# Optimization experiments

Hardware: AMD Instinct MI355X
Metric: run time of the kernel (lower is better)

Reference implementation:

```python
import jax, jax.numpy as jnp
from jax import lax
import numpy as np

KERNEL_SIZE = 5
GROUP_SIZE = 40
GMAX = 160                      # g sampled in [0, GMAX)
MAX_ITERS = (GMAX - 1) // GROUP_SIZE   # static upper bound on |g|//group_size = 3
B = 4096
D = 8192


def _circ_conv(x, k):
    # x: [1, B, D], k: [B, K] -> grouped (depthwise) circular conv1d, groups=B
    pad = KERNEL_SIZE - 1
    left = pad // 2
    xp = jnp.pad(x, ((0, 0), (0, 0), (left, pad - left)), mode='wrap')
    return lax.conv_general_dilated(
        xp, k[:, None, :], window_strides=(1,), padding='VALID',
        feature_group_count=k.shape[0], dimension_numbers=('NCH', 'OIH', 'NCH'))


def setup_inputs() -> dict:
    key = jax.random.key(0)
    k1, k2, k3 = jax.random.split(key, 3)
    x = jax.random.normal(k1, (B, D), dtype=jnp.float32)
    g = jax.random.randint(k2, (B,), 0, GMAX, dtype=jnp.int32)
    kernels = jax.random.normal(k3, (2 * GROUP_SIZE + 1, KERNEL_SIZE), dtype=jnp.float32)
    return {"x": x, "g": g, "kernels": kernels}


def reference(x, g, kernels):
    G = GROUP_SIZE
    xc = x[None]                          # [1, B, D]  (x.view(-1,1,D).permute(1,0,2))
    sign = jnp.sign(g)                    # [B]
    iters = jnp.abs(g) // G               # [B] data-dependent per-sample loop count
    max_it = jnp.max(iters)               # dynamic max over the batch
    max_k = kernels[sign * G + G]         # [B, K]
    id_k = kernels[G]                     # [K] learned 'identity' kernel
    # true delta kernel: exact no-op under circular pad, used for steps past max_it
    delta = jnp.zeros((KERNEL_SIZE,), x.dtype).at[(KERNEL_SIZE - 1) // 2].set(1.0)

    h = xc
    for i in range(MAX_ITERS):            # static bound; delta makes extra steps no-ops
        inactive = jnp.where(i < max_it, id_k, delta)          # [K]
        k_i = jnp.where((i < iters)[:, None], max_k, inactive[None, :])  # [B, K]
        h = _circ_conv(h, k_i)
    rem = jnp.abs(g) % G
    fin_k = kernels[rem * sign + G]       # [B, K]
    out = _circ_conv(h, fin_k)            # [1, B, D]
    return jnp.transpose(out, (1, 0, 2))  # [B, 1, D]
```

## Files before the change

kernel.cpp:

```cpp
#include <hip/hip_runtime.h>

#define BB 4096
#define DD 8192
#define KK 5
#define GS 40
#define MAXIT 3
#define EFF 17
#define CHUNK 2048
#define C4 (CHUNK/4)
#define DF4 (DD/4)

typedef float vf4 __attribute__((ext_vector_type(4)));

__device__ __forceinline__ int iabs(int a) { return a < 0 ? -a : a; }

__global__ __launch_bounds__(256) void k_max_it(const int* __restrict__ g,
                                                int* __restrict__ ws) {
    __shared__ int red[256];
    int t = threadIdx.x;
    int m = 0;
    for (int i = t; i < BB; i += 256) m = max(m, iabs(g[i]));
    red[t] = m;
    __syncthreads();
    for (int s = 128; s > 0; s >>= 1) {
        if (t < s) red[t] = max(red[t], red[t + s]);
        __syncthreads();
    }
    if (t == 0) ws[0] = red[0] / GS;
}

__global__ __launch_bounds__(256) void k_conv(const float* __restrict__ x,
                                              const int* __restrict__ g,
                                              const float* __restrict__ kernels,
                                              const int* __restrict__ ws,
                                              float* __restrict__ out) {
    __shared__ float lds[CHUNK + 16];
    float4* ldsv = (float4*)lds;

    const int bi   = blockIdx.x;
    const int b    = bi >> 2;
    const int ch   = bi & 3;
    const int t    = threadIdx.x;
    const int c0f4 = ch * C4;

    const float4* xr = (const float4*)(x + (size_t)b * DD);

    ldsv[2 + t]       = xr[c0f4 + t];
    ldsv[2 + t + 256] = xr[c0f4 + t + 256];
    if (t == 0) {
        ldsv[0] = xr[(c0f4 - 2) & (DF4 - 1)];
        ldsv[1] = xr[(c0f4 - 1) & (DF4 - 1)];
    } else if (t == 1) {
        ldsv[514] = xr[(c0f4 + C4)     & (DF4 - 1)];
        ldsv[515] = xr[(c0f4 + C4 + 1) & (DF4 - 1)];
    }

    const int gv    = g[b];
    const int sign  = gv > 0 ? 1 : (gv < 0 ? -1 : 0);
    const int a     = iabs(gv);
    const int iters = a / GS;
    const int rem   = a % GS;
    const int max_it = ws[0];

    float maxk[KK], idk[KK], fink[KK];
    const float* mk = kernels + (size_t)(sign * GS + GS) * KK;
    const float* ik = kernels + (size_t)GS * KK;
    const float* fk = kernels + (size_t)(rem * sign + GS) * KK;
#pragma unroll
    for (int j = 0; j < KK; ++j) { maxk[j] = mk[j]; idk[j] = ik[j]; fink[j] = fk[j]; }

    float e[EFF], ne[EFF];
#pragma unroll
    for (int m = 0; m < EFF; ++m) e[m] = 0.f;
    e[0] = 1.f;
    int len = 1;
    for (int i = 0; i < MAXIT; ++i) {
        float kk5[KK];
        if (i < iters) {
#pragma unroll
            for (int j = 0; j < KK; ++j) kk5[j] = maxk[j];
        } else if (i < max_it) {
#pragma unroll
            for (int j = 0; j < KK; ++j) kk5[j] = idk[j];
        } else {
#pragma unroll
            for (int j = 0; j < KK; ++j) kk5[j] = (j == (KK - 1) / 2) ? 1.f : 0.f;
        }
#pragma unroll
        for (int m = 0; m < EFF; ++m) ne[m] = 0.f;
        for (int m = 0; m < len; ++m)
#pragma unroll
            for (int j = 0; j < KK; ++j) ne[m + j] += e[m] * kk5[j];
        len += KK - 1;
#pragma unroll
        for (int m = 0; m < EFF; ++m) e[m] = ne[m];
    }
#pragma unroll
    for (int m = 0; m < EFF; ++m) ne[m] = 0.f;
    for (int m = 0; m < len; ++m)
#pragma unroll
        for (int j = 0; j < KK; ++j) ne[m + j] += e[m] * fink[j];
#pragma unroll
    for (int m = 0; m < EFF; ++m) e[m] = ne[m];

    __syncthreads();

    vf4* outr = (vf4*)(out + (size_t)b * DD);
#pragma unroll
    for (int jb = 0; jb < 2; ++jb) {
        const int v = jb * 256 + t;
        float f[EFF + 3];
#pragma unroll
        for (int q = 0; q < 5; ++q) {
            float4 val = ldsv[v + q];
            f[q * 4 + 0] = val.x; f[q * 4 + 1] = val.y;
            f[q * 4 + 2] = val.z; f[q * 4 + 3] = val.w;
        }
        float oc[4];
#pragma unroll
        for (int c = 0; c < 4; ++c) {
            float s = 0.f;
#pragma unroll
            for (int m = 0; m < EFF; ++m) s += e[m] * f[c + m];
            oc[c] = s;
        }
        vf4 o;
        o.x = oc[0]; o.y = oc[1]; o.z = oc[2]; o.w = oc[3];
        __builtin_nontemporal_store(o, outr + c0f4 + v);
    }
}

extern "C" void kernel_launch(void* const* d_in, const int* in_sizes, int n_in,
                              void* d_out, int out_size, void* d_ws, size_t ws_size,
                              hipStream_t stream) {
    const float* x       = (const float*)d_in[0];
    const int*   g       = (const int*)d_in[1];
    const float* kernels = (const float*)d_in[2];
    float*       out     = (float*)d_out;
    int*         ws      = (int*)d_ws;

    k_max_it<<<1, 256, 0, stream>>>(g, ws);
    k_conv<<<BB * (DD / CHUNK), 256, 0, stream>>>(x, g, kernels, ws, out);
}
```

Baseline: 236.8 us.

## Precompute composed per-row 17-tap kernels in a separate pass

Adds a small kernel that computes the batch max and each row's composed 17-tap filter once, writing the results to workspace. The main conv kernel then loads five float4 values instead of recomputing the filter composition in every one of the four chunk blocks per row. The loop-based composition is also replaced with fully unrolled fixed-length templates. The old path is kept as a fallback when the workspace is too small, and each of the 16 compose blocks redoes the full max reduction over g.

```diff
diff --git a/kernel.cpp b/kernel.cpp
--- a/kernel.cpp
+++ b/kernel.cpp
@@ -9,31 +9,92 @@
 #define CHUNK 2048
 #define C4 (CHUNK/4)
 #define DF4 (DD/4)
+#define EPAD 20
+#define WS_OFF 64
 
 typedef float vf4 __attribute__((ext_vector_type(4)));
 
 __device__ __forceinline__ int iabs(int a) { return a < 0 ? -a : a; }
 
-__global__ __launch_bounds__(256) void k_max_it(const int* __restrict__ g,
-                                                int* __restrict__ ws) {
+template<int LEN>
+__device__ __forceinline__ void compose5(float* e, const float* k5) {
+    float ne[LEN + KK - 1];
+#pragma unroll
+    for (int m = 0; m < LEN + KK - 1; ++m) ne[m] = 0.f;
+#pragma unroll
+    for (int m = 0; m < LEN; ++m)
+#pragma unroll
+        for (int j = 0; j < KK; ++j) ne[m + j] += e[m] * k5[j];
+#pragma unroll
+    for (int m = 0; m < LEN + KK - 1; ++m) e[m] = ne[m];
+}
+
+__device__ __forceinline__ void pick5(int i, int iters, int max_it,
+                                      const float* maxk, const float* idk,
+                                      float* k5) {
+#pragma unroll
+    for (int j = 0; j < KK; ++j)
+        k5[j] = (i < iters) ? maxk[j]
+              : ((i < max_it) ? idk[j] : ((j == (KK - 1) / 2) ? 1.f : 0.f));
+}
+
+__global__ __launch_bounds__(256) void k_compose(const int* __restrict__ g,
+                                                 const float* __restrict__ kernels,
+                                                 float* __restrict__ wsE) {
     __shared__ int red[256];
-    int t = threadIdx.x;
+    const int t = threadIdx.x;
+
+    const int4* g4 = (const int4*)g;
     int m = 0;
-    for (int i = t; i < BB; i += 256) m = max(m, iabs(g[i]));
+    for (int i = t; i < BB / 4; i += 256) {
+        int4 v = g4[i];
+        m = max(m, max(max(iabs(v.x), iabs(v.y)), max(iabs(v.z), iabs(v.w))));
+    }
     red[t] = m;
     __syncthreads();
     for (int s = 128; s > 0; s >>= 1) {
         if (t < s) red[t] = max(red[t], red[t + s]);
         __syncthreads();
     }
-    if (t == 0) ws[0] = red[0] / GS;
-}
-
-__global__ __launch_bounds__(256) void k_conv(const float* __restrict__ x,
-                                              const int* __restrict__ g,
-                                              const float* __restrict__ kernels,
-                                              const int* __restrict__ ws,
-                                              float* __restrict__ out) {
+    const int max_it = red[0] / GS;
+
+    const int r  = blockIdx.x * 256 + t;
+    const int gv = g[r];
+    const int sign  = gv > 0 ? 1 : (gv < 0 ? -1 : 0);
+    const int a     = iabs(gv);
+    const int iters = a / GS;
+    const int rem   = a % GS;
+
+    const float* mk = kernels + (size_t)(sign * GS + GS) * KK;
+    const float* ik = kernels + (size_t)GS * KK;
+    const float* fk = kernels + (size_t)(rem * sign + GS) * KK;
+    float maxk[KK], idk[KK], fink[KK];
+#pragma unroll
+    for (int j = 0; j < KK; ++j) { maxk[j] = mk[j]; idk[j] = ik[j]; fink[j] = fk[j]; }
+
+    float e[EPAD];
+#pragma unroll
+    for (int q = 0; q < EPAD; ++q) e[q] = 0.f;
+    e[0] = 1.f;
+
+    float k5[KK];
+    pick5(0, iters, max_it, maxk, idk, k5); compose5<1>(e, k5);
+    pick5(1, iters, max_it, maxk, idk, k5); compose5<5>(e, k5);
+    pick5(2, iters, max_it, maxk, idk, k5); compose5<9>(e, k5);
+    compose5<13>(e, fink);
+
+    vf4* dst = (vf4*)(wsE + (size_t)r * EPAD);
+    vf4 o0; o0.x = e[0];  o0.y = e[1];  o0.z = e[2];  o0.w = e[3];
+    vf4 o1; o1.x = e[4];  o1.y = e[5];  o1.z = e[6];  o1.w = e[7];
+    vf4 o2; o2.x = e[8];  o2.y = e[9];  o2.z = e[10]; o2.w = e[11];
+    vf4 o3; o3.x = e[12]; o3.y = e[13]; o3.z = e[14]; o3.w = e[15];
+    vf4 o4; o4.x = e[16]; o4.y = e[17]; o4.z = e[18]; o4.w = e[19];
+    dst[0] = o0; dst[1] = o1; dst[2] = o2; dst[3] = o3; dst[4] = o4;
+}
+
+__global__ __launch_bounds__(256) void k_conv_pre(const float* __restrict__ x,
+                                                  const float* __restrict__ wsE,
+                                                  float* __restrict__ out) {
     __shared__ float lds[CHUNK + 16];
     float4* ldsv = (float4*)lds;
 
@@ -55,6 +116,82 @@
         ldsv[515] = xr[(c0f4 + C4 + 1) & (DF4 - 1)];
     }
 
+    const float4* ev = (const float4*)(wsE + (size_t)b * EPAD);
+    float4 e0 = ev[0], e1 = ev[1], e2 = ev[2], e3 = ev[3], e4 = ev[4];
+    float e[EFF] = { e0.x, e0.y, e0.z, e0.w,
+                     e1.x, e1.y, e1.z, e1.w,
+                     e2.x, e2.y, e2.z, e2.w,
+                     e3.x, e3.y, e3.z, e3.w,
+                     e4.x };
+
+    __syncthreads();
+
+    vf4* outr = (vf4*)(out + (size_t)b * DD);
+#pragma unroll
+    for (int jb = 0; jb < 2; ++jb) {
+        const int v = jb * 256 + t;
+        float f[EFF + 3];
+#pragma unroll
+        for (int q = 0; q < 5; ++q) {
+            float4 val = ldsv[v + q];
+            f[q * 4 + 0] = val.x; f[q * 4 + 1] = val.y;
+            f[q * 4 + 2] = val.z; f[q * 4 + 3] = val.w;
+        }
+        float oc[4];
+#pragma unroll
+        for (int c = 0; c < 4; ++c) {
+            float s = 0.f;
+#pragma unroll
+            for (int m = 0; m < EFF; ++m) s += e[m] * f[c + m];
+            oc[c] = s;
+        }
+        vf4 o;
+        o.x = oc[0]; o.y = oc[1]; o.z = oc[2]; o.w = oc[3];
+        __builtin_nontemporal_store(o, outr + c0f4 + v);
+    }
+}
+
+__global__ __launch_bounds__(256) void k_max_it(const int* __restrict__ g,
+                                                int* __restrict__ ws) {
+    __shared__ int red[256];
+    int t = threadIdx.x;
+    int m = 0;
+    for (int i = t; i < BB; i += 256) m = max(m, iabs(g[i]));
+    red[t] = m;
+    __syncthreads();
+    for (int s = 128; s > 0; s >>= 1) {
+        if (t < s) red[t] = max(red[t], red[t + s]);
+        __syncthreads();
+    }
+    if (t == 0) ws[0] = red[0] / GS;
+}
+
+__global__ __launch_bounds__(256) void k_conv(const float* __restrict__ x,
+                                              const int* __restrict__ g,
+                                              const float* __restrict__ kernels,
+                                              const int* __restrict__ ws,
+                                              float* __restrict__ out) {
+    __shared__ float lds[CHUNK + 16];
+    float4* ldsv = (float4*)lds;
+
+    const int bi   = blockIdx.x;
+    const int b    = bi >> 2;
+    const int ch   = bi & 3;
+    const int t    = threadIdx.x;
+    const int c0f4 = ch * C4;
+
+    const float4* xr = (const float4*)(x + (size_t)b * DD);
+
+    ldsv[2 + t]       = xr[c0f4 + t];
+    ldsv[2 + t + 256] = xr[c0f4 + t + 256];
+    if (t == 0) {
+        ldsv[0] = xr[(c0f4 - 2) & (DF4 - 1)];
+        ldsv[1] = xr[(c0f4 - 1) & (DF4 - 1)];
+    } else if (t == 1) {
+        ldsv[514] = xr[(c0f4 + C4)     & (DF4 - 1)];
+        ldsv[515] = xr[(c0f4 + C4 + 1) & (DF4 - 1)];
+    }
+
     const int gv    = g[b];
     const int sign  = gv > 0 ? 1 : (gv < 0 ? -1 : 0);
     const int a     = iabs(gv);
@@ -69,39 +206,15 @@
 #pragma unroll
     for (int j = 0; j < KK; ++j) { maxk[j] = mk[j]; idk[j] = ik[j]; fink[j] = fk[j]; }
 
-    float e[EFF], ne[EFF];
-#pragma unroll
-    for (int m = 0; m < EFF; ++m) e[m] = 0.f;
+    float e[EPAD];
+#pragma unroll
+    for (int q = 0; q < EPAD; ++q) e[q] = 0.f;
     e[0] = 1.f;
-    int len = 1;
-    for (int i = 0; i < MAXIT; ++i) {
-        float kk5[KK];
-        if (i < iters) {
-#pragma unroll
-            for (int j = 0; j < KK; ++j) kk5[j] = maxk[j];
-        } else if (i < max_it) {
-#pragma unroll
-            for (int j = 0; j < KK; ++j) kk5[j] = idk[j];
-        } else {
-#pragma unroll
-            for (int j = 0; j < KK; ++j) kk5[j] = (j == (KK - 1) / 2) ? 1.f : 0.f;
-        }
-#pragma unroll
-        for (int m = 0; m < EFF; ++m) ne[m] = 0.f;
-        for (int m = 0; m < len; ++m)
-#pragma unroll
-            for (int j = 0; j < KK; ++j) ne[m + j] += e[m] * kk5[j];
-        len += KK - 1;
-#pragma unroll
-        for (int m = 0; m < EFF; ++m) e[m] = ne[m];
-    }
-#pragma unroll
-    for (int m = 0; m < EFF; ++m) ne[m] = 0.f;
-    for (int m = 0; m < len; ++m)
-#pragma unroll
-        for (int j = 0; j < KK; ++j) ne[m + j] += e[m] * fink[j];
-#pragma unroll
-    for (int m = 0; m < EFF; ++m) e[m] = ne[m];
+    float k5[KK];
+    pick5(0, iters, max_it, maxk, idk, k5); compose5<1>(e, k5);
+    pick5(1, iters, max_it, maxk, idk, k5); compose5<5>(e, k5);
+    pick5(2, iters, max_it, maxk, idk, k5); compose5<9>(e, k5);
+    compose5<13>(e, fink);
 
     __syncthreads();
 
@@ -137,8 +250,15 @@
     const int*   g       = (const int*)d_in[1];
     const float* kernels = (const float*)d_in[2];
     float*       out     = (float*)d_out;
-    int*         ws      = (int*)d_ws;
-
-    k_max_it<<<1, 256, 0, stream>>>(g, ws);
-    k_conv<<<BB * (DD / CHUNK), 256, 0, stream>>>(x, g, kernels, ws, out);
-}
+
+    const size_t need = (size_t)(WS_OFF + BB * EPAD) * sizeof(float);
+    if (ws_size >= need) {
+        float* wsE = (float*)d_ws + WS_OFF;
+        k_compose<<<BB / 256, 256, 0, stream>>>(g, kernels, wsE);
+        k_conv_pre<<<BB * (DD / CHUNK), 256, 0, stream>>>(x, wsE, out);
+    } else {
+        int* ws = (int*)d_ws;
+        k_max_it<<<1, 256, 0, stream>>>(g, ws);
+        k_conv<<<BB * (DD / CHUNK), 256, 0, stream>>>(x, g, kernels, ws, out);
+    }
+}
```

Result: no change. 235.8 us (-0.4%).
